# Performance work log

Hardware: AMD Instinct MI355X
Metric: run time of the kernel (lower is better)

Reference implementation:

```python
import jax, jax.numpy as jnp
import numpy as np
from jax import lax

STRIDE = 8  # backbone patch-embed stride


def setup_inputs() -> dict:
    key = jax.random.key(0)
    ks = jax.random.split(key, 5)
    B, H, W = 2, 256, 256
    Cr, Cg, Cout = 256, 5, 256
    N = 65536  # memory bank size
    return {
        "image": jax.random.normal(ks[0], (B, 3, H, W), dtype=jnp.float32),
        "geometry_map": jax.random.uniform(ks[1], (B, Cg, H, W), dtype=jnp.float32),
        "backbone_w": jax.random.normal(ks[2], (Cr, 3, STRIDE, STRIDE), dtype=jnp.float32) * 0.05,
        "backbone_b": jnp.zeros((Cr,), dtype=jnp.float32),
        "fusion_w": jax.random.normal(ks[3], (Cout, Cr + Cg), dtype=jnp.float32) * 0.05,
        "fusion_b": jnp.zeros((Cout,), dtype=jnp.float32),
        "memory_bank": jax.random.normal(ks[4], (N, Cout), dtype=jnp.float32),
    }


def reference(image, geometry_map, backbone_w, backbone_b, fusion_w, fusion_b, memory_bank):
    # --- backbone: patch-embed conv + relu -> (B,Cr,H',W') ---
    feat_rgb = lax.conv_general_dilated(
        image, backbone_w, window_strides=(STRIDE, STRIDE), padding="VALID",
        dimension_numbers=("NCHW", "OIHW", "NCHW"))
    feat_rgb = jax.nn.relu(feat_rgb + backbone_b[None, :, None, None])
    B, Cr, H, W = feat_rgb.shape

    # --- bilinear align of geometry map (align_corners=False semantics) ---
    geo = jax.image.resize(geometry_map, (B, geometry_map.shape[1], H, W), method="bilinear")

    # --- fusion 1x1 conv ---
    fused = jnp.concatenate([feat_rgb, geo], axis=1)           # (B, Cr+Cg, H, W)
    fused = jnp.einsum("oc,bchw->bohw", fusion_w, fused) + fusion_b[None, :, None, None]
    C = fused.shape[1]

    # --- NN min-distance to memory bank (cdist + min) ---
    flat = fused.transpose(0, 2, 3, 1).reshape(-1, C)          # (M, C)
    d2 = (jnp.sum(flat * flat, axis=1)[:, None]
          + jnp.sum(memory_bank * memory_bank, axis=1)[None, :]
          - 2.0 * flat @ memory_bank.T)                        # (M, N)
    min_dist = jnp.sqrt(jnp.maximum(jnp.min(d2, axis=1), 0.0))  # sqrt monotone: min before sqrt
    score_plain = min_dist.reshape(B, H, W)

    # --- geometry reweighting (sigmoid mode, alpha=1.0) ---
    density, opacity, anis = geo[:, 3:4], geo[:, 2:3], geo[:, 4:5]
    base = 0.5 * density + 0.25 * (1.0 - opacity) + 0.25 * anis
    w = 1.0 + jax.nn.sigmoid(4.0 * (base - 0.5))               # (B,1,H,W)
    score_geo = score_plain * w[:, 0]
    return score_plain, score_geo
```

## Files before the change

kernel.cpp:

```cpp
#include <hip/hip_runtime.h>
#include <hip/hip_bf16.h>
#include <stdint.h>

typedef __attribute__((ext_vector_type(8))) short bf16x8;
typedef __attribute__((ext_vector_type(4))) float f32x4;

#define NP 2048
#define NBANK 65536
#define NCHUNKS 32
#define CHUNK 2048
#define SUBR 64
#define NSUB 32
#define CF 261

__device__ inline short f2bf(float f) {
  __hip_bfloat16 h = __float2bfloat16(f);
  return *reinterpret_cast<short*>(&h);
}

__global__ __launch_bounds__(256) void k_repack_fw(
    const float* __restrict__ fw, float* __restrict__ fwp)
{
  int idx = blockIdx.x * 256 + threadIdx.x;
  int o = idx / 264, c = idx % 264;
  fwp[idx] = (c < CF) ? fw[(size_t)o * CF + c] : 0.f;
}

__global__ __launch_bounds__(512) void k_prep(
    const float* __restrict__ image, const float* __restrict__ geometry,
    const float* __restrict__ bw, const float* __restrict__ bb,
    const float* __restrict__ fwp, const float* __restrict__ fb,
    const float* __restrict__ mb,
    short* __restrict__ flatb, float* __restrict__ qsq, float* __restrict__ wgt,
    short* __restrict__ mbb, float* __restrict__ msq)
{
  __shared__ __align__(16) float patch[1536];
  __shared__ __align__(16) float fusedS[8][264];
  __shared__ float gv[40][8];
  __shared__ float gw[40][8];
  __shared__ float redS[8][8];
  int t = threadIdx.x;
  int bid = blockIdx.x;

  if (bid >= 256) {
    int row = (bid - 256) * 8 + (t >> 6);
    int lane = t & 63;
    float4 v = ((const float4*)(mb + (size_t)row * 256))[lane];
    short4 o; o.x = f2bf(v.x); o.y = f2bf(v.y); o.z = f2bf(v.z); o.w = f2bf(v.w);
    ((short4*)(mbb + (size_t)row * 256))[lane] = o;
    float s = v.x*v.x + v.y*v.y + v.z*v.z + v.w*v.w;
    #pragma unroll
    for (int m = 1; m < 64; m <<= 1) s += __shfl_xor(s, m);
    if (lane == 0) msq[row] = s;
    return;
  }

  int b = bid >> 7, rem = bid & 127, h = rem >> 2, w0 = (rem & 3) * 8;

  #pragma unroll
  for (int j = 0; j < 3; j++) {
    int idx = t + j * 512;
    int c = idx >> 9, r = (idx >> 6) & 7, col = idx & 63;
    patch[idx] = image[(((size_t)(b*3 + c) * 256) + 8*h + r) * 256 + 8*w0 + col];
  }
  if (t >= 320 && t < 344) {
    int i = (t - 320) / 3, c = 261 + (t - 320) % 3;
    fusedS[i][c] = 0.f;
  }
  if (t < 320) {
    int v = t >> 3, sub = t & 7;
    int i = v / 5, cg = v % 5;
    int jj = w0 + i;
    float val = 0.f, ws = 0.f;
    const float* gch = geometry + (size_t)(b*5 + cg) * 65536;
    #pragma unroll
    for (int rr = 0; rr < 2; rr++) {
      int r = sub * 2 + rr;
      int gr = 8*h - 4 + r;
      float wr = 1.f - fabsf((float)r - 7.5f) * 0.125f;
      if (gr >= 0 && gr < 256) {
        const float* grow = gch + (size_t)gr * 256;
        for (int c = 0; c < 16; c++) {
          int gc = 8*jj - 4 + c;
          if (gc >= 0 && gc < 256) {
            float wc_ = 1.f - fabsf((float)c - 7.5f) * 0.125f;
            val += wr * wc_ * grow[gc];
            ws  += wr * wc_;
          }
        }
      }
    }
    gv[v][sub] = val; gw[v][sub] = ws;
  }
  __syncthreads();
  if (t < 40) {
    int i = t / 5, cg = t % 5;
    float sv = 0.f, sw = 0.f;
    #pragma unroll
    for (int u = 0; u < 8; u++) { sv += gv[t][u]; sw += gw[t][u]; }
    fusedS[i][256 + cg] = sv / sw;
  }

  int g = t >> 8, o = t & 255;
  float a4[4] = {0.f, 0.f, 0.f, 0.f};
  const float4* wo4 = (const float4*)(bw + (size_t)o * 192);
  for (int cr = 0; cr < 24; cr++) {
    const float4* prow4 = (const float4*)&patch[cr * 64 + g * 32];
    float4 wA = wo4[cr*2], wB = wo4[cr*2 + 1];
    #pragma unroll
    for (int i4 = 0; i4 < 4; i4++) {
      float4 p0 = prow4[i4*2], p1 = prow4[i4*2 + 1];
      a4[i4] += wA.x*p0.x + wA.y*p0.y + wA.z*p0.z + wA.w*p0.w
              + wB.x*p1.x + wB.y*p1.y + wB.z*p1.z + wB.w*p1.w;
    }
  }
  float bias = bb[o];
  #pragma unroll
  for (int i4 = 0; i4 < 4; i4++) fusedS[g*4 + i4][o] = fmaxf(a4[i4] + bias, 0.f);
  __syncthreads();

  #pragma unroll
  for (int i4 = 0; i4 < 4; i4++) a4[i4] = 0.f;
  const float4* fwo4 = (const float4*)(fwp + (size_t)o * 264);
  for (int c4 = 0; c4 < 66; c4++) {
    float4 w4 = fwo4[c4];
    #pragma unroll
    for (int i4 = 0; i4 < 4; i4++) {
      float4 f4 = *(const float4*)&fusedS[g*4 + i4][c4*4];
      a4[i4] += w4.x*f4.x + w4.y*f4.y + w4.z*f4.z + w4.w*f4.w;
    }
  }
  float fbias = fb[o];
  int lane = t & 63, wid = t >> 6;
  #pragma unroll
  for (int i4 = 0; i4 < 4; i4++) {
    a4[i4] += fbias;
    int p = b*1024 + h*32 + w0 + g*4 + i4;
    flatb[(size_t)p * 256 + o] = f2bf(a4[i4]);
    float s = a4[i4] * a4[i4];
    #pragma unroll
    for (int m = 1; m < 64; m <<= 1) s += __shfl_xor(s, m);
    if (lane == 0) redS[g*4 + i4][wid & 3] = s;
  }
  __syncthreads();
  if (t < 8) {
    float s = redS[t][0] + redS[t][1] + redS[t][2] + redS[t][3];
    int p = b*1024 + h*32 + w0 + t;
    qsq[p] = s;
    float den = fusedS[t][256+3], opa = fusedS[t][256+2], ani = fusedS[t][256+4];
    float base2 = 0.5f*den + 0.25f*(1.f - opa) + 0.25f*ani;
    wgt[p] = 1.f + 1.f/(1.f + expf(-4.f*(base2 - 0.5f)));
  }
}

__global__ __launch_bounds__(256, 2) void k_distmin(
    const short* __restrict__ Aq, const short* __restrict__ Bb,
    const float* __restrict__ qsq, const float* __restrict__ msq,
    float* __restrict__ partial)
{
  __shared__ __align__(16) unsigned char sB[2][32768];
  __shared__ float red[2][128];
  int t = threadIdx.x;
  int lane = t & 63, wid = t >> 6;
  int wr = wid >> 1, wc = wid & 1;
  const int l15 = lane & 15, l4 = lane >> 4;
  int nc = blockIdx.x, mt = blockIdx.y;
  int m0 = mt * 128;
  const size_t nchunk0 = (size_t)nc * CHUNK;
  const unsigned char* Bbyte = (const unsigned char*)Bb + nchunk0 * 512;
  const unsigned char* Abyte = (const unsigned char*)Aq;

  int soff[8];
  #pragma unroll
  for (int j = 0; j < 8; j++) {
    int sh = j * 4 + wid;
    int ks = sh & 7, hh = (sh >> 3) & 1, wcs = sh >> 4;
    soff[j] = (wcs * 32 + hh * 16 + l15) * 512 + ks * 64 + l4 * 16;
  }

  bf16x8 af[4][8];
  #pragma unroll
  for (int mi = 0; mi < 4; mi++)
    #pragma unroll
    for (int ks = 0; ks < 8; ks++)
      af[mi][ks] = *(const bf16x8*)(Abyte +
          (size_t)(m0 + wr*64 + mi*16 + l15) * 512 + ks*64 + l4*16);

  float vmin[4][4];
  #pragma unroll
  for (int mi = 0; mi < 4; mi++)
    #pragma unroll
    for (int r = 0; r < 4; r++) vmin[mi][r] = 3.4e38f;

#define STAGE(bufsel, sidx) do {                                              \
    const unsigned char* gb_ = Bbyte + (size_t)(sidx) * 32768;                \
    unsigned char* lb_ = &sB[bufsel][0] + wid * 1024;                         \
    _Pragma("unroll")                                                         \
    for (int j_ = 0; j_ < 8; j_++) {                                          \
      __builtin_amdgcn_global_load_lds(                                       \
        (const __attribute__((address_space(1))) unsigned int*)(gb_ + soff[j_]), \
        (__attribute__((address_space(3))) unsigned int*)(lb_ + j_*4096),     \
        16, 0, 0);                                                            \
    }                                                                         \
  } while (0)

  STAGE(0, 0);
  __syncthreads();

  int cur = 0;
  for (int s = 0; s < NSUB; s++) {
    if (s + 1 < NSUB) STAGE(cur ^ 1, s + 1);
    const size_t nb = nchunk0 + (size_t)s * SUBR;
    float msq0 = msq[nb + wc * 32 + l15];
    float msq1 = msq[nb + wc * 32 + 16 + l15];
    const unsigned char* buf = &sB[cur][0] + wc * 16384;

    f32x4 acc[4][2];
    #pragma unroll
    for (int mi = 0; mi < 4; mi++) {
      acc[mi][0] = (f32x4){0.f, 0.f, 0.f, 0.f};
      acc[mi][1] = (f32x4){0.f, 0.f, 0.f, 0.f};
    }
    #pragma unroll
    for (int ks = 0; ks < 8; ks++) {
      bf16x8 b0 = *(const bf16x8*)(buf + ks*1024 + l4*256 + l15*16);
      bf16x8 b1 = *(const bf16x8*)(buf + 8192 + ks*1024 + l4*256 + l15*16);
      #pragma unroll
      for (int mi = 0; mi < 4; mi++) {
        acc[mi][0] = __builtin_amdgcn_mfma_f32_16x16x32_bf16(af[mi][ks], b0, acc[mi][0], 0, 0, 0);
        acc[mi][1] = __builtin_amdgcn_mfma_f32_16x16x32_bf16(af[mi][ks], b1, acc[mi][1], 0, 0, 0);
      }
    }
    #pragma unroll
    for (int mi = 0; mi < 4; mi++)
      #pragma unroll
      for (int r = 0; r < 4; r++) {
        float v = fminf(msq0 - 2.f*acc[mi][0][r], msq1 - 2.f*acc[mi][1][r]);
        vmin[mi][r] = fminf(vmin[mi][r], v);
      }
    __syncthreads();
    cur ^= 1;
  }
#undef STAGE

  #pragma unroll
  for (int mi = 0; mi < 4; mi++)
    #pragma unroll
    for (int r = 0; r < 4; r++) {
      float v = vmin[mi][r];
      v = fminf(v, __shfl_xor(v, 1));
      v = fminf(v, __shfl_xor(v, 2));
      v = fminf(v, __shfl_xor(v, 4));
      v = fminf(v, __shfl_xor(v, 8));
      if (l15 == 0) red[wc][wr * 64 + mi * 16 + l4 * 4 + r] = v;
    }
  __syncthreads();
  if (t < 128) {
    float v = fminf(red[0][t], red[1][t]);
    float d2 = qsq[m0 + t] + v;
    partial[(size_t)(m0 + t) * NCHUNKS + nc] = fmaxf(d2, 0.f);
  }
}

__global__ __launch_bounds__(256) void k_final(
    const float* __restrict__ partial, const float* __restrict__ wgt,
    float* __restrict__ out)
{
  int q = blockIdx.x * 256 + threadIdx.x;
  const float4* p = (const float4*)(partial + (size_t)q * NCHUNKS);
  float v = 3.4e38f;
  #pragma unroll
  for (int j = 0; j < 8; j++) {
    float4 x = p[j];
    v = fminf(v, fminf(fminf(x.x, x.y), fminf(x.z, x.w)));
  }
  float sp = sqrtf(v);
  out[q] = sp;
  out[NP + q] = sp * wgt[q];
}

extern "C" void kernel_launch(void* const* d_in, const int* in_sizes, int n_in,
                              void* d_out, int out_size, void* d_ws, size_t ws_size,
                              hipStream_t stream) {
  const float* image    = (const float*)d_in[0];
  const float* geometry = (const float*)d_in[1];
  const float* bw       = (const float*)d_in[2];
  const float* bb       = (const float*)d_in[3];
  const float* fw       = (const float*)d_in[4];
  const float* fb       = (const float*)d_in[5];
  const float* mb       = (const float*)d_in[6];
  float* out = (float*)d_out;
  char* ws = (char*)d_ws;

  float* wgt     = (float*)(ws);
  float* qsq     = (float*)(ws + 8192);
  float* msq     = (float*)(ws + 16384);
  float* fwp     = (float*)(ws + 278528);
  short* flatb   = (short*)(ws + 548864);
  float* partial = (float*)(ws + 1597440);
  short* mbb     = (short*)(ws + 1859584);

  hipLaunchKernelGGL(k_repack_fw, dim3(264),     dim3(256), 0, stream, fw, fwp);
  hipLaunchKernelGGL(k_prep,      dim3(8448),    dim3(512), 0, stream,
                     image, geometry, bw, bb, fwp, fb, mb, flatb, qsq, wgt, mbb, msq);
  hipLaunchKernelGGL(k_distmin,   dim3(32, 16),  dim3(256), 0, stream, flatb, mbb, qsq, msq, partial);
  hipLaunchKernelGGL(k_final,     dim3(8),       dim3(256), 0, stream, partial, wgt, out);
}
```

Baseline: 221.5 us.

## Pre-swizzle bf16 memory bank into LDS tile order during prep

The prep kernel now converts the memory bank to bf16 and stores it in the exact order the distance kernel's LDS staging expects. It goes through a 32KB shared-memory transpose per 64-row block and then issues fully contiguous 16-byte stores. The distance kernel's async global-to-LDS loads then become contiguous per wave (wid*1024 + lane*16 + j*4096) instead of strided gathers, which removes the per-thread offset table and improves coalescing. Prep uses fewer, larger blocks (1024 bank blocks of 64 rows instead of 8192 of 8), and the bank now carries a layout that only k_distmin understands.

```diff
diff --git a/kernel.cpp b/kernel.cpp
--- a/kernel.cpp
+++ b/kernel.cpp
@@ -34,26 +34,43 @@
     short* __restrict__ flatb, float* __restrict__ qsq, float* __restrict__ wgt,
     short* __restrict__ mbb, float* __restrict__ msq)
 {
-  __shared__ __align__(16) float patch[1536];
-  __shared__ __align__(16) float fusedS[8][264];
-  __shared__ float gv[40][8];
-  __shared__ float gw[40][8];
-  __shared__ float redS[8][8];
+  __shared__ __align__(16) unsigned char shmem[32768];
   int t = threadIdx.x;
   int bid = blockIdx.x;
 
   if (bid >= 256) {
-    int row = (bid - 256) * 8 + (t >> 6);
-    int lane = t & 63;
-    float4 v = ((const float4*)(mb + (size_t)row * 256))[lane];
-    short4 o; o.x = f2bf(v.x); o.y = f2bf(v.y); o.z = f2bf(v.z); o.w = f2bf(v.w);
-    ((short4*)(mbb + (size_t)row * 256))[lane] = o;
-    float s = v.x*v.x + v.y*v.y + v.z*v.z + v.w*v.w;
-    #pragma unroll
-    for (int m = 1; m < 64; m <<= 1) s += __shfl_xor(s, m);
-    if (lane == 0) msq[row] = s;
+    int s = bid - 256;
+    int r = t >> 3, q = t & 7;
+    int wcs = r >> 5, hh = (r >> 4) & 1, l15r = r & 15;
+    const float* src = mb + ((size_t)s * 64 + r) * 256;
+    float s2 = 0.f;
+    #pragma unroll
+    for (int i = 0; i < 8; i++) {
+      float4 v = *(const float4*)(src + q * 4 + i * 32);
+      short4 o; o.x = f2bf(v.x); o.y = f2bf(v.y); o.z = f2bf(v.z); o.w = f2bf(v.w);
+      int kbyte = q * 8 + i * 64;
+      int ks = kbyte >> 6, l4 = (kbyte >> 4) & 3, b8 = kbyte & 8;
+      int c = wcs * 16 + hh * 8 + ks;
+      *(short4*)(shmem + c * 1024 + l4 * 256 + l15r * 16 + b8) = o;
+      s2 += v.x * v.x + v.y * v.y + v.z * v.z + v.w * v.w;
+    }
+    s2 += __shfl_xor(s2, 1); s2 += __shfl_xor(s2, 2); s2 += __shfl_xor(s2, 4);
+    if (q == 0) msq[(size_t)s * 64 + r] = s2;
+    __syncthreads();
+    unsigned char* dstg = (unsigned char*)mbb + (size_t)s * 32768;
+    #pragma unroll
+    for (int i = 0; i < 4; i++) {
+      int S = t + i * 512;
+      *(float4*)(dstg + S * 16) = *(const float4*)(shmem + S * 16);
+    }
     return;
   }
+
+  float* patch = (float*)shmem;
+  float (*fusedS)[264] = (float (*)[264])(shmem + 6144);
+  float (*gv)[8] = (float (*)[8])(shmem + 14592);
+  float (*gw)[8] = (float (*)[8])(shmem + 15872);
+  float (*redS)[8] = (float (*)[8])(shmem + 17152);
 
   int b = bid >> 7, rem = bid & 127, h = rem >> 2, w0 = (rem & 3) * 8;
 
@@ -170,14 +187,6 @@
   const unsigned char* Bbyte = (const unsigned char*)Bb + nchunk0 * 512;
   const unsigned char* Abyte = (const unsigned char*)Aq;
 
-  int soff[8];
-  #pragma unroll
-  for (int j = 0; j < 8; j++) {
-    int sh = j * 4 + wid;
-    int ks = sh & 7, hh = (sh >> 3) & 1, wcs = sh >> 4;
-    soff[j] = (wcs * 32 + hh * 16 + l15) * 512 + ks * 64 + l4 * 16;
-  }
-
   bf16x8 af[4][8];
   #pragma unroll
   for (int mi = 0; mi < 4; mi++)
@@ -193,12 +202,12 @@
     for (int r = 0; r < 4; r++) vmin[mi][r] = 3.4e38f;
 
 #define STAGE(bufsel, sidx) do {                                              \
-    const unsigned char* gb_ = Bbyte + (size_t)(sidx) * 32768;                \
+    const unsigned char* gb_ = Bbyte + (size_t)(sidx) * 32768 + wid * 1024 + lane * 16; \
     unsigned char* lb_ = &sB[bufsel][0] + wid * 1024;                         \
     _Pragma("unroll")                                                         \
     for (int j_ = 0; j_ < 8; j_++) {                                          \
       __builtin_amdgcn_global_load_lds(                                       \
-        (const __attribute__((address_space(1))) unsigned int*)(gb_ + soff[j_]), \
+        (const __attribute__((address_space(1))) unsigned int*)(gb_ + j_*4096), \
         (__attribute__((address_space(3))) unsigned int*)(lb_ + j_*4096),     \
         16, 0, 0);                                                            \
     }                                                                         \
@@ -301,7 +310,7 @@
   short* mbb     = (short*)(ws + 1859584);
 
   hipLaunchKernelGGL(k_repack_fw, dim3(264),     dim3(256), 0, stream, fw, fwp);
-  hipLaunchKernelGGL(k_prep,      dim3(8448),    dim3(512), 0, stream,
+  hipLaunchKernelGGL(k_prep,      dim3(1280),    dim3(512), 0, stream,
                      image, geometry, bw, bb, fwp, fb, mb, flatb, qsq, wgt, mbb, msq);
   hipLaunchKernelGGL(k_distmin,   dim3(32, 16),  dim3(256), 0, stream, flatb, mbb, qsq, msq, partial);
   hipLaunchKernelGGL(k_final,     dim3(8),       dim3(256), 0, stream, partial, wgt, out);
```

Result: faster. 199.2 us (-10.1%).
